# Kernel tuning notes

Hardware: AMD Instinct MI355X
Metric: run time of the kernel (lower is better)

Reference implementation:

```python
import jax, jax.numpy as jnp
import numpy as np

N, M_NODES, E_EDGES, D = 32, 128, 256, 128  # note: D must equal M_NODES (see original convK1 constraint)


def setup_inputs() -> dict:
    key = jax.random.key(0)
    k1, k2, k3, k4, k5 = jax.random.split(key, 5)
    feature_matrix = jax.random.normal(k1, (N, M_NODES, D), dtype=jnp.float32)
    incidence_matrix = (jax.random.uniform(k2, (N, M_NODES, E_EDGES)) < 0.25).astype(jnp.float32)
    # grouped Conv1d(m, m*m, d, groups=m) weights reshaped to (m, m, d); bias (m, m)
    Wkk = jax.random.normal(k3, (M_NODES, M_NODES, D), dtype=jnp.float32) * (1.0 / np.sqrt(D))
    bkk = jax.random.normal(k4, (M_NODES, M_NODES), dtype=jnp.float32) * 0.01
    # Conv1d(m, 1, 1) weights: (1, m, 1) -> vector of length m (== d)
    w1 = jax.random.normal(k5, (D,), dtype=jnp.float32) * (1.0 / np.sqrt(D))
    b1 = jnp.zeros((), dtype=jnp.float32)
    return {"feature_matrix": feature_matrix, "incidence_matrix": incidence_matrix,
            "Wkk": Wkk, "bkk": bkk, "w1": w1, "b1": b1}


def reference(feature_matrix, incidence_matrix, Wkk, bkk, w1, b1):
    n, m, d = feature_matrix.shape
    e = incidence_matrix.shape[-1]
    # incidence broadcast: (N,m,1,d) * (N,m,e,1) -> (N,m,e,d) -> (N,e,m,d) -> (N*e, m, d)
    region = feature_matrix[:, :, None, :] * incidence_matrix[:, :, :, None]
    region = region.transpose(0, 2, 1, 3).reshape(n * e, m, d)
    # grouped conv with full-length kernel == per-row dot products
    logits = jnp.einsum('bid,ijd->bij', region, Wkk) + bkk  # (B, m, m)
    multiplier = jax.nn.softmax(logits, axis=-1)
    transformed = jax.nn.relu(jnp.einsum('bij,bjd->bid', multiplier, region))  # (B, m, d)
    # Conv1d(m,1,1) on (B, d, m): weighted sum over the feature axis (valid since d == m)
    pooled = jnp.einsum('bld,d->bl', transformed, w1) + b1  # (B, m) with m == d
    return pooled.reshape(n, e, d)
```

## Files before the change

kernel.cpp:

```cpp
#include <hip/hip_runtime.h>

#define NN 32
#define MM 128
#define EE 256
#define DD 128
#define ELB 32

typedef __attribute__((ext_vector_type(8))) short short8;
typedef __attribute__((ext_vector_type(4))) float f32x4;

union U16x8 { uint4 u; short8 s; };

static __device__ __forceinline__ unsigned short f2bf(float f) {
  union { float f; unsigned u; } v; v.f = f;
  unsigned r = v.u + 0x7FFFu + ((v.u >> 16) & 1u);
  return (unsigned short)(r >> 16);
}

__global__ __launch_bounds__(256, 1)
void k_pre(const float* __restrict__ X, const float* __restrict__ inc,
           const float* __restrict__ Wkk, const float* __restrict__ bkk,
           unsigned short* __restrict__ P1g, unsigned short* __restrict__ P0g,
           unsigned short* __restrict__ XTg, unsigned* __restrict__ bmap) {
  __shared__ float xs[64][129];
  const int bid = blockIdx.x;
  const int t = threadIdx.x;

  if (bid < 64) {
    const int i  = bid * 2 + (t >> 7);
    const int tt = t & 127;
    const int ty = tt >> 6;
    const int l  = tt & 63;
    const int lr = l & 15, lg = l >> 4;

    short8 a[4];
    {
      const int n = ty * 16 + lr;
      const float* xp = X + (n * MM + i) * DD + lg * 8;
#pragma unroll
      for (int k = 0; k < 4; ++k) {
        float4 v0 = *(const float4*)(xp + k * 32);
        float4 v1 = *(const float4*)(xp + k * 32 + 4);
        short8 s;
        s[0]=(short)f2bf(v0.x); s[1]=(short)f2bf(v0.y); s[2]=(short)f2bf(v0.z); s[3]=(short)f2bf(v0.w);
        s[4]=(short)f2bf(v1.x); s[5]=(short)f2bf(v1.y); s[6]=(short)f2bf(v1.z); s[7]=(short)f2bf(v1.w);
        a[k] = s;
      }
    }
    f32x4 acc[8];
#pragma unroll
    for (int cf = 0; cf < 8; ++cf) acc[cf] = (f32x4){0.f, 0.f, 0.f, 0.f};
#pragma unroll
    for (int k = 0; k < 4; ++k) {
#pragma unroll
      for (int cf = 0; cf < 8; ++cf) {
        const int j = cf * 16 + lr;
        const float* wp = Wkk + (i * MM + j) * DD + k * 32 + lg * 8;
        float4 v0 = *(const float4*)(wp);
        float4 v1 = *(const float4*)(wp + 4);
        short8 b;
        b[0]=(short)f2bf(v0.x); b[1]=(short)f2bf(v0.y); b[2]=(short)f2bf(v0.z); b[3]=(short)f2bf(v0.w);
        b[4]=(short)f2bf(v1.x); b[5]=(short)f2bf(v1.y); b[6]=(short)f2bf(v1.z); b[7]=(short)f2bf(v1.w);
        acc[cf] = __builtin_amdgcn_mfma_f32_16x16x32_bf16(a[k], b, acc[cf], 0, 0, 0);
      }
    }
    float bk[8];
#pragma unroll
    for (int cf = 0; cf < 8; ++cf) bk[cf] = bkk[i * MM + cf * 16 + lr];
#pragma unroll
    for (int r = 0; r < 4; ++r) {
      float v[8], m = -1e30f;
#pragma unroll
      for (int cf = 0; cf < 8; ++cf) { v[cf] = acc[cf][r] + bk[cf]; m = fmaxf(m, v[cf]); }
#pragma unroll
      for (int s = 1; s < 16; s <<= 1) m = fmaxf(m, __shfl_xor(m, s, 64));
      float sum = 0.f;
#pragma unroll
      for (int cf = 0; cf < 8; ++cf) { v[cf] = __expf(v[cf] - m); sum += v[cf]; }
#pragma unroll
      for (int s = 1; s < 16; s <<= 1) sum += __shfl_xor(sum, s, 64);
      const float inv = 1.f / sum;
      const int n = ty * 16 + lg * 4 + r;
      unsigned short* dst = P1g + (n * MM + i) * MM;
#pragma unroll
      for (int cf = 0; cf < 8; ++cf) dst[cf * 16 + lr] = f2bf(v[cf] * inv);
    }
    if (ty == 0) {
      float v0 = bkk[i * MM + l], v1 = bkk[i * MM + 64 + l];
      float m = fmaxf(v0, v1);
#pragma unroll
      for (int s = 1; s < 64; s <<= 1) m = fmaxf(m, __shfl_xor(m, s, 64));
      v0 = __expf(v0 - m); v1 = __expf(v1 - m);
      float sum = v0 + v1;
#pragma unroll
      for (int s = 1; s < 64; s <<= 1) sum += __shfl_xor(sum, s, 64);
      const float inv = 1.f / sum;
      P0g[i * MM + l]      = f2bf(v0 * inv);
      P0g[i * MM + 64 + l] = f2bf(v1 * inv);
    }
  } else if (bid < 128) {
    const int idx = bid - 64;
    const int n = idx >> 1, jh = idx & 1;
#pragma unroll
    for (int it = 0; it < 8; ++it) {
      int id2 = it * 256 + t;
      int j = id2 >> 5, dq = id2 & 31;
      float4 v = *(const float4*)(X + (n * MM + jh * 64 + j) * DD + dq * 4);
      xs[j][dq * 4 + 0] = v.x; xs[j][dq * 4 + 1] = v.y;
      xs[j][dq * 4 + 2] = v.z; xs[j][dq * 4 + 3] = v.w;
    }
    __syncthreads();
    const int d = t >> 1, half = t & 1;
    unsigned* dst = (unsigned*)XTg + (n * DD + d) * (MM / 2) + jh * 32 + half * 16;
#pragma unroll
    for (int wq = 0; wq < 16; ++wq) {
      int jl = half * 32 + wq * 2;
      unsigned u0 = f2bf(xs[jl][d]), u1 = f2bf(xs[jl + 1][d]);
      dst[wq] = u0 | (u1 << 16);
    }
  } else {
    const int idx = bid - 128;
    const int n = idx >> 2, q = idx & 3;
    const int e = t;
    unsigned bm = 0;
#pragma unroll 4
    for (int j = 0; j < 32; ++j)
      if (inc[(n * MM + q * 32 + j) * EE + e] != 0.f) bm |= 1u << j;
    bmap[(n * EE + e) * 4 + q] = bm;
  }
}

__global__ __launch_bounds__(256, 2)
void k_main(const unsigned short* __restrict__ P0g, const unsigned short* __restrict__ P1g,
            const unsigned short* __restrict__ XTg, const unsigned* __restrict__ bmap,
            const float* __restrict__ w1, const float* __restrict__ b1p,
            float* __restrict__ out) {
  __shared__ unsigned bitm[ELB][4];
  __shared__ alignas(16) unsigned short mrow[ELB][128];

  const int bid = blockIdx.x;
  const int n = bid & 31, eg = (bid >> 5) & 7, rh = bid >> 8;
  const int t = threadIdx.x, w = t >> 6, l = t & 63, lr = l & 15, lg = l >> 4;
  const int i_lane = rh * 64 + w * 16 + lr;

  if (t < ELB)
    *(uint4*)&bitm[t][0] = *(const uint4*)(bmap + (n * EE + eg * ELB + t) * 4);

  uint4 x[8][4];
  {
    const unsigned short* xb = XTg + n * DD * MM;
#pragma unroll
    for (int cf = 0; cf < 8; ++cf)
#pragma unroll
      for (int k = 0; k < 4; ++k)
        x[cf][k] = *(const uint4*)(xb + (cf * 16 + lr) * MM + k * 32 + lg * 8);
  }
  uint4 p0[4], p1[4];
  {
    const unsigned short* pb0 = P0g + i_lane * MM;
    const unsigned short* pb1 = P1g + n * MM * MM + i_lane * MM;
#pragma unroll
    for (int k = 0; k < 4; ++k) {
      p0[k] = *(const uint4*)(pb0 + k * 32 + lg * 8);
      p1[k] = *(const uint4*)(pb1 + k * 32 + lg * 8);
    }
  }
  U16x8 w1u[4];
#pragma unroll
  for (int p = 0; p < 4; ++p) {
    float4 a = *(const float4*)(w1 + (2 * p) * 16 + lg * 4);
    float4 b = *(const float4*)(w1 + (2 * p + 1) * 16 + lg * 4);
    short8 s;
    s[0]=(short)f2bf(a.x); s[1]=(short)f2bf(a.y); s[2]=(short)f2bf(a.z); s[3]=(short)f2bf(a.w);
    s[4]=(short)f2bf(b.x); s[5]=(short)f2bf(b.y); s[6]=(short)f2bf(b.z); s[7]=(short)f2bf(b.w);
    w1u[p].s = s;
  }
#pragma unroll
  for (int cf = 0; cf < 8; ++cf) {
#pragma unroll
    for (int k = 0; k < 4; ++k)
      asm volatile("" : "+v"(x[cf][k].x), "+v"(x[cf][k].y), "+v"(x[cf][k].z), "+v"(x[cf][k].w));
  }
#pragma unroll
  for (int k = 0; k < 4; ++k) {
    asm volatile("" : "+v"(p0[k].x), "+v"(p0[k].y), "+v"(p0[k].z), "+v"(p0[k].w));
    asm volatile("" : "+v"(p1[k].x), "+v"(p1[k].y), "+v"(p1[k].z), "+v"(p1[k].w));
    asm volatile("" : "+v"(w1u[k].u.x), "+v"(w1u[k].u.y), "+v"(w1u[k].u.z), "+v"(w1u[k].u.w));
  }
  const float b1v = b1p[0];
  const int selsh = (w & 1) * 16 + lr;
  const int selwd = rh * 2 + (w >> 1);
  __syncthreads();

  {
    int el = t >> 3, j0 = (t & 7) * 16;
    unsigned wd = bitm[el][j0 >> 5];
    int sh = j0 & 31;
    unsigned short* mp = &mrow[el][j0];
#pragma unroll
    for (int b = 0; b < 16; ++b) mp[b] = ((wd >> (sh + b)) & 1u) ? 0xFFFFu : 0u;
  }
  __syncthreads();

  unsigned selbits = 0;
#pragma unroll
  for (int el = 0; el < ELB; ++el)
    selbits |= ((bitm[el][selwd] >> selsh) & 1u) << el;

  float* outp = out + (n * EE + eg * ELB) * MM + rh * 64 + w * 16 + lg * 4;
  const char* mbase = (const char*)&mrow[0][0] + lg * 16;

  uint4 mmN[4];
#pragma unroll
  for (int k = 0; k < 4; ++k) mmN[k] = *(const uint4*)(mbase + k * 64);

#pragma unroll 1
  for (int el = 0; el < ELB; ++el) {
    uint4 mmv[4];
#pragma unroll
    for (int k = 0; k < 4; ++k) mmv[k] = mmN[k];
    {
      const int eln = (el + 1 < ELB) ? (el + 1) : el;
      const char* mb = mbase + eln * 256;
#pragma unroll
      for (int k = 0; k < 4; ++k) mmN[k] = *(const uint4*)(mb + k * 64);
    }
    const bool sel = ((selbits >> el) & 1u) != 0u;

    U16x8 pv[4];
#pragma unroll
    for (int k = 0; k < 4; ++k) {
      pv[k].u.x = (sel ? p1[k].x : p0[k].x) & mmv[k].x;
      pv[k].u.y = (sel ? p1[k].y : p0[k].y) & mmv[k].y;
      pv[k].u.z = (sel ? p1[k].z : p0[k].z) & mmv[k].z;
      pv[k].u.w = (sel ? p1[k].w : p0[k].w) & mmv[k].w;
    }

    f32x4 eA = (f32x4){b1v, b1v, b1v, b1v};
#pragma unroll
    for (int p = 0; p < 4; ++p) {
      f32x4 a0v = (f32x4){0.f,0.f,0.f,0.f}, a1v = (f32x4){0.f,0.f,0.f,0.f};
#pragma unroll
      for (int k = 0; k < 4; ++k) {
        U16x8 xv0; xv0.u = x[2*p][k];
        U16x8 xv1; xv1.u = x[2*p+1][k];
        a0v = __builtin_amdgcn_mfma_f32_16x16x32_bf16(xv0.s, pv[k].s, a0v, 0, 0, 0);
        a1v = __builtin_amdgcn_mfma_f32_16x16x32_bf16(xv1.s, pv[k].s, a1v, 0, 0, 0);
      }
      float f0 = fmaxf(a0v[0],0.f), f1 = fmaxf(a0v[1],0.f), f2 = fmaxf(a0v[2],0.f), f3 = fmaxf(a0v[3],0.f);
      float g0 = fmaxf(a1v[0],0.f), g1 = fmaxf(a1v[1],0.f), g2 = fmaxf(a1v[2],0.f), g3 = fmaxf(a1v[3],0.f);
      unsigned u0,u1,u2,u3;
      asm("v_cvt_pk_bf16_f32 %0, %1, %2" : "=v"(u0) : "v"(f0), "v"(f1));
      asm("v_cvt_pk_bf16_f32 %0, %1, %2" : "=v"(u1) : "v"(f2), "v"(f3));
      asm("v_cvt_pk_bf16_f32 %0, %1, %2" : "=v"(u2) : "v"(g0), "v"(g1));
      asm("v_cvt_pk_bf16_f32 %0, %1, %2" : "=v"(u3) : "v"(g2), "v"(g3));
      U16x8 uu; uu.u.x = u0; uu.u.y = u1; uu.u.z = u2; uu.u.w = u3;
      eA = __builtin_amdgcn_mfma_f32_16x16x32_bf16(uu.s, w1u[p].s, eA, 0, 0, 0);
    }

    if (lr == 0) *(float4*)(outp + el * MM) = *(float4*)&eA;
  }
}

extern "C" void kernel_launch(void* const* d_in, const int* in_sizes, int n_in,
                              void* d_out, int out_size, void* d_ws, size_t ws_size,
                              hipStream_t stream) {
  const float* X   = (const float*)d_in[0];
  const float* inc = (const float*)d_in[1];
  const float* Wkk = (const float*)d_in[2];
  const float* bkk = (const float*)d_in[3];
  const float* w1  = (const float*)d_in[4];
  const float* b1  = (const float*)d_in[5];
  float* out = (float*)d_out;

  unsigned short* P1g = (unsigned short*)d_ws;
  unsigned short* XTg = P1g + NN * MM * DD;
  unsigned short* P0g = XTg + NN * MM * DD;
  unsigned* bmap = (unsigned*)(P0g + MM * MM);

  hipLaunchKernelGGL(k_pre,  dim3(256), dim3(256), 0, stream, X, inc, Wkk, bkk, P1g, P0g, XTg, bmap);
  hipLaunchKernelGGL(k_main, dim3(512), dim3(256), 0, stream, P0g, P1g, XTg, bmap, w1, b1, out);
}
```

Baseline: 53.60 us.

## Use hardware bf16 pack conversion, split pooling accumulator, drop manual mask prefetch

Replaces the software round-to-nearest bf16 conversion with the v_cvt_pk_bf16_f32 instruction in the precompute and setup paths. In the main loop, the pooling MFMA accumulation is split across two accumulators to shorten the dependent chain. The register-held mask prefetch is replaced by direct LDS loads, with the loop unrolled by two so the compiler can overlap them. Together these are meant to cut conversion ALU work, MFMA dependency stalls and register pressure, at the risk of exposing LDS latency.

```diff
diff --git a/kernel.cpp b/kernel.cpp
--- a/kernel.cpp
+++ b/kernel.cpp
@@ -15,6 +15,15 @@
   union { float f; unsigned u; } v; v.f = f;
   unsigned r = v.u + 0x7FFFu + ((v.u >> 16) & 1u);
   return (unsigned short)(r >> 16);
+}
+
+static __device__ __forceinline__ U16x8 pk8(float4 a, float4 b) {
+  U16x8 r;
+  asm("v_cvt_pk_bf16_f32 %0, %1, %2" : "=v"(r.u.x) : "v"(a.x), "v"(a.y));
+  asm("v_cvt_pk_bf16_f32 %0, %1, %2" : "=v"(r.u.y) : "v"(a.z), "v"(a.w));
+  asm("v_cvt_pk_bf16_f32 %0, %1, %2" : "=v"(r.u.z) : "v"(b.x), "v"(b.y));
+  asm("v_cvt_pk_bf16_f32 %0, %1, %2" : "=v"(r.u.w) : "v"(b.z), "v"(b.w));
+  return r;
 }
 
 __global__ __launch_bounds__(256, 1)
@@ -41,10 +50,7 @@
       for (int k = 0; k < 4; ++k) {
         float4 v0 = *(const float4*)(xp + k * 32);
         float4 v1 = *(const float4*)(xp + k * 32 + 4);
-        short8 s;
-        s[0]=(short)f2bf(v0.x); s[1]=(short)f2bf(v0.y); s[2]=(short)f2bf(v0.z); s[3]=(short)f2bf(v0.w);
-        s[4]=(short)f2bf(v1.x); s[5]=(short)f2bf(v1.y); s[6]=(short)f2bf(v1.z); s[7]=(short)f2bf(v1.w);
-        a[k] = s;
+        a[k] = pk8(v0, v1).s;
       }
     }
     f32x4 acc[8];
@@ -58,10 +64,7 @@
         const float* wp = Wkk + (i * MM + j) * DD + k * 32 + lg * 8;
         float4 v0 = *(const float4*)(wp);
         float4 v1 = *(const float4*)(wp + 4);
-        short8 b;
-        b[0]=(short)f2bf(v0.x); b[1]=(short)f2bf(v0.y); b[2]=(short)f2bf(v0.z); b[3]=(short)f2bf(v0.w);
-        b[4]=(short)f2bf(v1.x); b[5]=(short)f2bf(v1.y); b[6]=(short)f2bf(v1.z); b[7]=(short)f2bf(v1.w);
-        acc[cf] = __builtin_amdgcn_mfma_f32_16x16x32_bf16(a[k], b, acc[cf], 0, 0, 0);
+        acc[cf] = __builtin_amdgcn_mfma_f32_16x16x32_bf16(a[k], pk8(v0, v1).s, acc[cf], 0, 0, 0);
       }
     }
     float bk[8];
@@ -115,8 +118,9 @@
 #pragma unroll
     for (int wq = 0; wq < 16; ++wq) {
       int jl = half * 32 + wq * 2;
-      unsigned u0 = f2bf(xs[jl][d]), u1 = f2bf(xs[jl + 1][d]);
-      dst[wq] = u0 | (u1 << 16);
+      unsigned u;
+      asm("v_cvt_pk_bf16_f32 %0, %1, %2" : "=v"(u) : "v"(xs[jl][d]), "v"(xs[jl + 1][d]));
+      dst[wq] = u;
     }
   } else {
     const int idx = bid - 128;
@@ -170,10 +174,7 @@
   for (int p = 0; p < 4; ++p) {
     float4 a = *(const float4*)(w1 + (2 * p) * 16 + lg * 4);
     float4 b = *(const float4*)(w1 + (2 * p + 1) * 16 + lg * 4);
-    short8 s;
-    s[0]=(short)f2bf(a.x); s[1]=(short)f2bf(a.y); s[2]=(short)f2bf(a.z); s[3]=(short)f2bf(a.w);
-    s[4]=(short)f2bf(b.x); s[5]=(short)f2bf(b.y); s[6]=(short)f2bf(b.z); s[7]=(short)f2bf(b.w);
-    w1u[p].s = s;
+    w1u[p] = pk8(a, b);
   }
 #pragma unroll
   for (int cf = 0; cf < 8; ++cf) {
@@ -210,33 +211,22 @@
   float* outp = out + (n * EE + eg * ELB) * MM + rh * 64 + w * 16 + lg * 4;
   const char* mbase = (const char*)&mrow[0][0] + lg * 16;
 
-  uint4 mmN[4];
-#pragma unroll
-  for (int k = 0; k < 4; ++k) mmN[k] = *(const uint4*)(mbase + k * 64);
-
-#pragma unroll 1
+#pragma unroll 2
   for (int el = 0; el < ELB; ++el) {
-    uint4 mmv[4];
-#pragma unroll
-    for (int k = 0; k < 4; ++k) mmv[k] = mmN[k];
-    {
-      const int eln = (el + 1 < ELB) ? (el + 1) : el;
-      const char* mb = mbase + eln * 256;
-#pragma unroll
-      for (int k = 0; k < 4; ++k) mmN[k] = *(const uint4*)(mb + k * 64);
-    }
     const bool sel = ((selbits >> el) & 1u) != 0u;
 
     U16x8 pv[4];
 #pragma unroll
     for (int k = 0; k < 4; ++k) {
-      pv[k].u.x = (sel ? p1[k].x : p0[k].x) & mmv[k].x;
-      pv[k].u.y = (sel ? p1[k].y : p0[k].y) & mmv[k].y;
-      pv[k].u.z = (sel ? p1[k].z : p0[k].z) & mmv[k].z;
-      pv[k].u.w = (sel ? p1[k].w : p0[k].w) & mmv[k].w;
-    }
-
-    f32x4 eA = (f32x4){b1v, b1v, b1v, b1v};
+      uint4 mm = *(const uint4*)(mbase + el * 256 + k * 64);
+      pv[k].u.x = (sel ? p1[k].x : p0[k].x) & mm.x;
+      pv[k].u.y = (sel ? p1[k].y : p0[k].y) & mm.y;
+      pv[k].u.z = (sel ? p1[k].z : p0[k].z) & mm.z;
+      pv[k].u.w = (sel ? p1[k].w : p0[k].w) & mm.w;
+    }
+
+    f32x4 e0 = (f32x4){b1v, b1v, b1v, b1v};
+    f32x4 e1 = (f32x4){0.f, 0.f, 0.f, 0.f};
 #pragma unroll
     for (int p = 0; p < 4; ++p) {
       f32x4 a0v = (f32x4){0.f,0.f,0.f,0.f}, a1v = (f32x4){0.f,0.f,0.f,0.f};
@@ -255,10 +245,14 @@
       asm("v_cvt_pk_bf16_f32 %0, %1, %2" : "=v"(u2) : "v"(g0), "v"(g1));
       asm("v_cvt_pk_bf16_f32 %0, %1, %2" : "=v"(u3) : "v"(g2), "v"(g3));
       U16x8 uu; uu.u.x = u0; uu.u.y = u1; uu.u.z = u2; uu.u.w = u3;
-      eA = __builtin_amdgcn_mfma_f32_16x16x32_bf16(uu.s, w1u[p].s, eA, 0, 0, 0);
-    }
-
-    if (lr == 0) *(float4*)(outp + el * MM) = *(float4*)&eA;
+      if (p & 1)
+        e1 = __builtin_amdgcn_mfma_f32_16x16x32_bf16(uu.s, w1u[p].s, e1, 0, 0, 0);
+      else
+        e0 = __builtin_amdgcn_mfma_f32_16x16x32_bf16(uu.s, w1u[p].s, e0, 0, 0, 0);
+    }
+    e0[0] += e1[0]; e0[1] += e1[1]; e0[2] += e1[2]; e0[3] += e1[3];
+
+    if (lr == 0) *(float4*)(outp + el * MM) = *(float4*)&e0;
   }
 }
 
```

After: 53.39 us. No clear change (-0.4%).
